# Optimization experiments

Hardware: AMD Instinct MI355X
Metric: run time of the kernel (lower is better)

The kernel has to match this reference:

```python
import jax, jax.numpy as jnp
import numpy as np

N_NODES = 102400   # 256 graphs x 400 nodes
N_EDGES = 1638400  # avg degree 16
C_IN = 128
C_OUT = 128
N_SAGE = 3         # gnn_num
G = 256            # num graphs
M = 400            # nodes per graph (equal-sized -> to_dense_batch is a reshape)


def setup_inputs() -> dict:
    key = jax.random.key(0)
    ks = jax.random.split(key, 6)
    x = jax.random.normal(ks[0], (N_NODES, C_IN), dtype=jnp.float32)
    edge_index = jax.random.randint(ks[1], (2, N_EDGES), 0, N_NODES, dtype=jnp.int32)
    # nodes sorted by graph id, equal graph sizes (matches to_dense_batch assumptions)
    batch = (jnp.arange(N_NODES, dtype=jnp.int32) // M)
    s_in = 1.0 / np.sqrt(C_IN)
    s_out = 1.0 / np.sqrt(C_OUT)
    W_g = jax.random.normal(ks[2], (C_IN, C_OUT), dtype=jnp.float32) * s_in
    b_g = jnp.zeros((C_OUT,), dtype=jnp.float32)
    W_l = jax.random.normal(ks[3], (N_SAGE, C_OUT, C_OUT), dtype=jnp.float32) * s_out  # neighbor lin
    b_l = jnp.zeros((N_SAGE, C_OUT), dtype=jnp.float32)
    W_r = jax.random.normal(ks[4], (N_SAGE, C_OUT, C_OUT), dtype=jnp.float32) * s_out  # root lin (no bias in PyG)
    return {"x": x, "W_g": W_g, "b_g": b_g, "W_l": W_l, "b_l": b_l,
            "W_r": W_r, "edge_index": edge_index, "batch": batch}


def _gcn_conv(x, W, b, src, dst):
    # PyG GCNConv: h = x W; add self loops; norm = d^{-1/2}_src * d^{-1/2}_dst,
    # deg = in-degree at dst counting the self loop; aggregate at dst; add bias.
    h = x @ W                                                     # [N, C_out]
    ones = jnp.ones((N_EDGES,), dtype=h.dtype)
    deg = jax.ops.segment_sum(ones, dst, num_segments=N_NODES) + 1.0
    dinv = jax.lax.rsqrt(deg)                                     # [N]
    norm = dinv[src] * dinv[dst]                                  # [E]
    agg = jax.ops.segment_sum(h[src] * norm[:, None], dst, num_segments=N_NODES)
    agg = agg + h * (dinv * dinv)[:, None]                        # self-loop term
    return agg + b


def _sage_conv(x, W_l, b_l, W_r, src, dst):
    # PyG SAGEConv (mean aggr): out = mean_{j in N(i)} x_j @ W_l + b_l + x @ W_r
    ones = jnp.ones((N_EDGES,), dtype=x.dtype)
    cnt = jax.ops.segment_sum(ones, dst, num_segments=N_NODES)
    s = jax.ops.segment_sum(x[src], dst, num_segments=N_NODES)
    mean = s / jnp.maximum(cnt, 1.0)[:, None]
    return mean @ W_l + b_l + x @ W_r


def _to_dense(x):
    # equal-sized graphs with nodes sorted by batch -> to_dense_batch == reshape
    return x.reshape(G, M, C_OUT)


def reference(x, W_g, b_g, W_l, b_l, W_r, edge_index, batch):
    src, dst = edge_index[0], edge_index[1]
    x = jax.nn.relu(_gcn_conv(x, W_g, b_g, src, dst))
    outs = [_to_dense(x)]
    for i in range(N_SAGE):
        x = jax.nn.relu(_sage_conv(x, W_l[i], b_l[i], W_r[i], src, dst))
        outs.append(_to_dense(x))
    return jnp.stack(outs)  # [N_SAGE+1, G, M, C_OUT]
```

## Files before the change

kernel.cpp:

```cpp
#include <hip/hip_runtime.h>

#define C 128
#define SLOT 64
typedef __attribute__((ext_vector_type(8))) short bf16x8;
typedef __attribute__((ext_vector_type(4))) float f32x4;

__device__ __forceinline__ unsigned short f2bf_rtn(float f) {
    unsigned u = __float_as_uint(f);
    return (unsigned short)((u + 0x7fff + ((u >> 16) & 1)) >> 16);
}
__device__ __forceinline__ float bflo(unsigned u) { return __uint_as_float(u << 16); }
__device__ __forceinline__ float bfhi(unsigned u) { return __uint_as_float(u & 0xffff0000u); }

__device__ __forceinline__ void gload_lds16(const unsigned short* g, unsigned short* l) {
    __builtin_amdgcn_global_load_lds(
        (const __attribute__((address_space(1))) void*)g,
        (__attribute__((address_space(3))) void*)l, 16, 0, 0);
}

__device__ __forceinline__ void split_bf16(float w, unsigned short& hb, unsigned short& lb) {
    unsigned u = __float_as_uint(w);
    hb = (unsigned short)(u >> 16);
    float hf = __uint_as_float(u & 0xffff0000u);
    lb = (unsigned short)(__float_as_uint(w - hf) >> 16);
}

__global__ __launch_bounds__(256) void wprep_all(const float* __restrict__ Wg,
        const float* __restrict__ Wl, const float* __restrict__ Wr,
        unsigned short* __restrict__ dstG, unsigned short* __restrict__ dstF) {
    int idx = blockIdx.x * 256 + threadIdx.x;
    if (idx < 16384) {
        int k64 = idx & 63, ch = (idx >> 6) & 127, chunk = idx >> 13;
        int k = chunk * 64 + k64;
        unsigned short hb, lb;
        split_bf16(Wg[(size_t)k * 128 + ch], hb, lb);
        int pos = (((k64 >> 3) ^ (ch & 7)) << 3) | (k64 & 7);
        size_t base = ((size_t)chunk * 2) * 8192 + ch * 64 + pos;
        dstG[base] = hb;
        dstG[base + 8192] = lb;
        return;
    }
    idx -= 16384;
    if (idx >= 3 * 4 * 128 * 64) return;
    int k64 = idx & 63, ch = (idx >> 6) & 127, chunk = (idx >> 13) & 3, layer = idx >> 15;
    int k = chunk * 64 + k64;
    float w = (k < 128) ? Wl[((size_t)layer * 128 + k) * 128 + ch]
                        : Wr[((size_t)layer * 128 + (k - 128)) * 128 + ch];
    unsigned short hb, lb;
    split_bf16(w, hb, lb);
    int pos = (((k64 >> 3) ^ (ch & 7)) << 3) | (k64 & 7);
    size_t base = (((size_t)layer * 4 + chunk) * 2) * 8192 + ch * 64 + pos;
    dstF[base] = hb;
    dstF[base + 8192] = lb;
}

__global__ __launch_bounds__(256) void build_gemm_kernel(
        const int* __restrict__ ei, int* __restrict__ deg, int* __restrict__ rank, int E,
        const float* __restrict__ x, const unsigned short* __restrict__ Wp,
        unsigned short* __restrict__ outbf) {
    __shared__ unsigned short Bs[2][128][64];
    const int b2 = blockIdx.x >> 1;
    const int t = threadIdx.x;

    if (!(blockIdx.x & 1)) {
        const int base = b2 * 1024 + t * 4;
        int4 d4 = *(const int4*)(ei + E + base);
        int4 r;
        r.x = atomicAdd(&deg[d4.x], 1);
        r.y = atomicAdd(&deg[d4.y], 1);
        r.z = atomicAdd(&deg[d4.z], 1);
        r.w = atomicAdd(&deg[d4.w], 1);
        *(int4*)(rank + base) = r;
        return;
    }

    unsigned short* BsFlat = &Bs[0][0][0];
    const int lane = t & 63;
    const int wv = t >> 6;
    const int rowbase = b2 * 64 + wv * 16;
    const int arow = rowbase + (lane & 15);
    const int kq = lane >> 4;

    f32x4 acc[8];
#pragma unroll
    for (int f = 0; f < 8; f++) acc[f] = (f32x4){0.f, 0.f, 0.f, 0.f};

#pragma unroll
    for (int c = 0; c < 2; c++) {
        __syncthreads();
        {
            const unsigned short* srcW = Wp + (size_t)c * 16384;
#pragma unroll
            for (int i = 0; i < 8; i++)
                gload_lds16(srcW + (wv * 8 + i) * 512 + lane * 8,
                            BsFlat + (wv * 8 + i) * 512);
        }
        bf16x8 Ah[2], Al[2];
#pragma unroll
        for (int j = 0; j < 2; j++) {
            const float* base = x + (size_t)arow * C + c * 64 + j * 32;
            float4 x0 = ((const float4*)base)[kq * 2];
            float4 x1 = ((const float4*)base)[kq * 2 + 1];
            float xv[8] = {x0.x, x0.y, x0.z, x0.w, x1.x, x1.y, x1.z, x1.w};
#pragma unroll
            for (int q = 0; q < 8; q++) {
                unsigned u = __float_as_uint(xv[q]);
                Ah[j][q] = (short)(u >> 16);
                float hf = __uint_as_float(u & 0xffff0000u);
                Al[j][q] = (short)(__float_as_uint(xv[q] - hf) >> 16);
            }
        }
        __syncthreads();
#pragma unroll
        for (int j = 0; j < 2; j++) {
#pragma unroll
            for (int f = 0; f < 8; f++) {
                const int chh = f * 16 + (lane & 15);
                const int uu = (j * 4 + kq) ^ (lane & 7);
                bf16x8 bh = *(const bf16x8*)&Bs[0][chh][uu * 8];
                bf16x8 bl = *(const bf16x8*)&Bs[1][chh][uu * 8];
                acc[f] = __builtin_amdgcn_mfma_f32_16x16x32_bf16(Ah[j], bh, acc[f], 0, 0, 0);
                acc[f] = __builtin_amdgcn_mfma_f32_16x16x32_bf16(Al[j], bh, acc[f], 0, 0, 0);
                acc[f] = __builtin_amdgcn_mfma_f32_16x16x32_bf16(Ah[j], bl, acc[f], 0, 0, 0);
            }
        }
    }
    const int col = lane & 15;
    const int rq = lane >> 4;
#pragma unroll
    for (int f = 0; f < 8; f++)
#pragma unroll
        for (int j = 0; j < 4; j++) {
            const size_t o = (size_t)(rowbase + rq * 4 + j) * C + f * 16 + col;
            outbf[o] = f2bf_rtn(acc[f][j]);
        }
}

__global__ __launch_bounds__(256) void scatter_scale_kernel(
        const int* __restrict__ ei, const int* __restrict__ rank,
        int* __restrict__ csr, int E, const int* __restrict__ deg,
        unsigned short* __restrict__ tbl, float* __restrict__ dinv,
        float* __restrict__ cinv, int n) {
    const int SB = E >> 10;
    const int t = threadIdx.x;
    if (blockIdx.x < SB) {
        const int base = blockIdx.x * 1024 + t * 4;
        int4 s4 = *(const int4*)(ei + base);
        int4 d4 = *(const int4*)(ei + E + base);
        int4 r4 = *(const int4*)(rank + base);
        if (r4.x < SLOT) csr[(d4.x << 6) + r4.x] = s4.x;
        if (r4.y < SLOT) csr[(d4.y << 6) + r4.y] = s4.y;
        if (r4.z < SLOT) csr[(d4.z << 6) + r4.z] = s4.z;
        if (r4.w < SLOT) csr[(d4.w << 6) + r4.w] = s4.w;
        return;
    }
    const int rb = (blockIdx.x - SB) * 16 + (t >> 4);
    if (rb >= n) return;
    const int ch = (t & 15) * 8;
    const int d = deg[rb];
    const float di = rsqrtf((float)(d + 1));
    if ((t & 15) == 0) {
        dinv[rb] = di;
        cinv[rb] = 1.0f / (float)max(d, 1);
    }
    unsigned short* row = tbl + (size_t)rb * C + ch;
    uint4 v = *(const uint4*)row;
    uint4 w;
    w.x = (unsigned)f2bf_rtn(bflo(v.x) * di) | ((unsigned)f2bf_rtn(bfhi(v.x) * di) << 16);
    w.y = (unsigned)f2bf_rtn(bflo(v.y) * di) | ((unsigned)f2bf_rtn(bfhi(v.y) * di) << 16);
    w.z = (unsigned)f2bf_rtn(bflo(v.z) * di) | ((unsigned)f2bf_rtn(bfhi(v.z) * di) << 16);
    w.w = (unsigned)f2bf_rtn(bflo(v.w) * di) | ((unsigned)f2bf_rtn(bfhi(v.w) * di) << 16);
    *(uint4*)row = w;
}

template<int WBF>
__global__ __launch_bounds__(256) void gemm_sage(
        const unsigned short* __restrict__ Xbf, const unsigned short* __restrict__ Mbf,
        const unsigned short* __restrict__ Wp, const float* __restrict__ bias,
        float* __restrict__ outf, unsigned short* __restrict__ outbf) {
    __shared__ unsigned short Bs[2][128][64];
    unsigned short* BsFlat = &Bs[0][0][0];
    const int t = threadIdx.x;
    const int lane = t & 63;
    const int wv = t >> 6;
    const int rowbase = blockIdx.x * 64 + wv * 16;
    const int arow = rowbase + (lane & 15);
    const int kq = lane >> 4;

    f32x4 acc[8];
#pragma unroll
    for (int f = 0; f < 8; f++) acc[f] = (f32x4){0.f, 0.f, 0.f, 0.f};

#pragma unroll
    for (int c = 0; c < 4; c++) {
        __syncthreads();
        {
            const unsigned short* srcW = Wp + (size_t)c * 16384;
#pragma unroll
            for (int i = 0; i < 8; i++)
                gload_lds16(srcW + (wv * 8 + i) * 512 + lane * 8,
                            BsFlat + (wv * 8 + i) * 512);
        }
        const unsigned short* tab = (c < 2) ? Mbf : Xbf;
        bf16x8 Ah[2];
#pragma unroll
        for (int j = 0; j < 2; j++)
            Ah[j] = *(const bf16x8*)(tab + (size_t)arow * C + (c & 1) * 64 + j * 32 + kq * 8);
        __syncthreads();
#pragma unroll
        for (int j = 0; j < 2; j++) {
#pragma unroll
            for (int f = 0; f < 8; f++) {
                const int chh = f * 16 + (lane & 15);
                const int uu = (j * 4 + kq) ^ (lane & 7);
                bf16x8 bh = *(const bf16x8*)&Bs[0][chh][uu * 8];
                bf16x8 bl = *(const bf16x8*)&Bs[1][chh][uu * 8];
                acc[f] = __builtin_amdgcn_mfma_f32_16x16x32_bf16(Ah[j], bh, acc[f], 0, 0, 0);
                acc[f] = __builtin_amdgcn_mfma_f32_16x16x32_bf16(Ah[j], bl, acc[f], 0, 0, 0);
            }
        }
    }
    const int col = lane & 15;
    const int rq = lane >> 4;
#pragma unroll
    for (int f = 0; f < 8; f++) {
        const float b = bias[f * 16 + col];
#pragma unroll
        for (int j = 0; j < 4; j++) {
            const size_t o = (size_t)(rowbase + rq * 4 + j) * C + f * 16 + col;
            float v = fmaxf(acc[f][j] + b, 0.f);
            outf[o] = v;
            if (WBF) outbf[o] = f2bf_rtn(v);
        }
    }
}

template<int SELF, int BIASRELU, int WF, int WBF>
__global__ __launch_bounds__(256) void agg_kernel(
        const unsigned short* __restrict__ tbl, const int* __restrict__ csr,
        const int* __restrict__ deg, const float* __restrict__ scale,
        const float* __restrict__ bias, float* __restrict__ outf,
        unsigned short* __restrict__ outbf, int n) {
    const int lane = threadIdx.x & 63;
    const int half = lane >> 5, li = lane & 31;
    const int i = blockIdx.x * 8 + (threadIdx.x >> 6) * 2 + half;
    if (i >= n) return;
    const int dcount = min(deg[i], SLOT);
    const int b = i << 6;
    const int c4 = li * 4;
    float a0 = 0.f, a1 = 0.f, a2 = 0.f, a3 = 0.f;
    for (int base = 0; base < dcount; base += 32) {
        const int cnt = min(32, dcount - base);
        int idx = (base + li < dcount) ? csr[b + base + li] : 0;
        int p = 0;
        for (; p + 8 <= cnt; p += 8) {
            int s0 = __shfl(idx, half * 32 + p);
            int s1 = __shfl(idx, half * 32 + p + 1);
            int s2 = __shfl(idx, half * 32 + p + 2);
            int s3 = __shfl(idx, half * 32 + p + 3);
            int s4 = __shfl(idx, half * 32 + p + 4);
            int s5 = __shfl(idx, half * 32 + p + 5);
            int s6 = __shfl(idx, half * 32 + p + 6);
            int s7 = __shfl(idx, half * 32 + p + 7);
            uint2 v0 = *(const uint2*)(tbl + (size_t)s0 * C + c4);
            uint2 v1 = *(const uint2*)(tbl + (size_t)s1 * C + c4);
            uint2 v2 = *(const uint2*)(tbl + (size_t)s2 * C + c4);
            uint2 v3 = *(const uint2*)(tbl + (size_t)s3 * C + c4);
            uint2 v4 = *(const uint2*)(tbl + (size_t)s4 * C + c4);
            uint2 v5 = *(const uint2*)(tbl + (size_t)s5 * C + c4);
            uint2 v6 = *(const uint2*)(tbl + (size_t)s6 * C + c4);
            uint2 v7 = *(const uint2*)(tbl + (size_t)s7 * C + c4);
            a0 += bflo(v0.x) + bflo(v1.x) + bflo(v2.x) + bflo(v3.x)
                + bflo(v4.x) + bflo(v5.x) + bflo(v6.x) + bflo(v7.x);
            a1 += bfhi(v0.x) + bfhi(v1.x) + bfhi(v2.x) + bfhi(v3.x)
                + bfhi(v4.x) + bfhi(v5.x) + bfhi(v6.x) + bfhi(v7.x);
            a2 += bflo(v0.y) + bflo(v1.y) + bflo(v2.y) + bflo(v3.y)
                + bflo(v4.y) + bflo(v5.y) + bflo(v6.y) + bflo(v7.y);
            a3 += bfhi(v0.y) + bfhi(v1.y) + bfhi(v2.y) + bfhi(v3.y)
                + bfhi(v4.y) + bfhi(v5.y) + bfhi(v6.y) + bfhi(v7.y);
        }
        for (; p + 4 <= cnt; p += 4) {
            int s0 = __shfl(idx, half * 32 + p);
            int s1 = __shfl(idx, half * 32 + p + 1);
            int s2 = __shfl(idx, half * 32 + p + 2);
            int s3 = __shfl(idx, half * 32 + p + 3);
            uint2 v0 = *(const uint2*)(tbl + (size_t)s0 * C + c4);
            uint2 v1 = *(const uint2*)(tbl + (size_t)s1 * C + c4);
            uint2 v2 = *(const uint2*)(tbl + (size_t)s2 * C + c4);
            uint2 v3 = *(const uint2*)(tbl + (size_t)s3 * C + c4);
            a0 += bflo(v0.x) + bflo(v1.x) + bflo(v2.x) + bflo(v3.x);
            a1 += bfhi(v0.x) + bfhi(v1.x) + bfhi(v2.x) + bfhi(v3.x);
            a2 += bflo(v0.y) + bflo(v1.y) + bflo(v2.y) + bflo(v3.y);
            a3 += bfhi(v0.y) + bfhi(v1.y) + bfhi(v2.y) + bfhi(v3.y);
        }
        for (; p < cnt; p++) {
            int s = __shfl(idx, half * 32 + p);
            uint2 v = *(const uint2*)(tbl + (size_t)s * C + c4);
            a0 += bflo(v.x); a1 += bfhi(v.x);
            a2 += bflo(v.y); a3 += bfhi(v.y);
        }
    }
    if (SELF) {
        uint2 h = *(const uint2*)(tbl + (size_t)i * C + c4);
        a0 += bflo(h.x); a1 += bfhi(h.x);
        a2 += bflo(h.y); a3 += bfhi(h.y);
    }
    const float sc = scale[i];
    a0 *= sc; a1 *= sc; a2 *= sc; a3 *= sc;
    if (BIASRELU) {
        float4 bb = *(const float4*)(bias + c4);
        a0 = fmaxf(a0 + bb.x, 0.f);
        a1 = fmaxf(a1 + bb.y, 0.f);
        a2 = fmaxf(a2 + bb.z, 0.f);
        a3 = fmaxf(a3 + bb.w, 0.f);
    }
    if (WF) {
        float4 r; r.x = a0; r.y = a1; r.z = a2; r.w = a3;
        *(float4*)(outf + (size_t)i * C + c4) = r;
    }
    if (WBF) {
        uint2 pk;
        pk.x = (unsigned)f2bf_rtn(a0) | ((unsigned)f2bf_rtn(a1) << 16);
        pk.y = (unsigned)f2bf_rtn(a2) | ((unsigned)f2bf_rtn(a3) << 16);
        *(uint2*)(outbf + (size_t)i * C + c4) = pk;
    }
}


extern "C" void kernel_launch(void* const* d_in, const int* in_sizes, int n_in,
                              void* d_out, int out_size, void* d_ws, size_t ws_size,
                              hipStream_t stream) {
    const float* x   = (const float*)d_in[0];
    const float* W_g = (const float*)d_in[1];
    const float* b_g = (const float*)d_in[2];
    const float* W_l = (const float*)d_in[3];
    const float* b_l = (const float*)d_in[4];
    const float* W_r = (const float*)d_in[5];
    const int*   ei  = (const int*)d_in[6];

    const int N = in_sizes[0] / C;
    const int E = in_sizes[6] / 2;
    const size_t NC = (size_t)N * C;

    char* ws = (char*)d_ws;
    unsigned short* meanbf = (unsigned short*)ws;
    int* rank = (int*)meanbf;
    unsigned short* tblA   = meanbf + NC;
    unsigned short* tblB   = tblA + NC;
    int* deg  = (int*)(tblB + NC);
    float* dinv = (float*)(deg + N);
    float* cinv = dinv + N;
    unsigned short* wsWg = (unsigned short*)(cinv + N);
    unsigned short* wsWf = wsWg + 32768;

    float* out0 = (float*)d_out;
    int* csr = (int*)(out0 + 3 * NC);

    hipMemsetAsync(deg, 0, (size_t)N * 4, stream);
    wprep_all<<<448, 256, 0, stream>>>(W_g, W_l, W_r, wsWg, wsWf);

    build_gemm_kernel<<<2 * (N / 64), 256, 0, stream>>>(ei, deg, rank, E,
                                                        x, wsWg, tblA);
    scatter_scale_kernel<<<(E >> 10) + N / 16, 256, 0, stream>>>(
        ei, rank, csr, E, deg, tblA, dinv, cinv, N);

    agg_kernel<1, 1, 1, 1><<<(N + 7) / 8, 256, 0, stream>>>(tblA, csr, deg, dinv,
                                                            b_g, out0, tblB, N);

    const unsigned short* tin[3] = {tblB, tblA, tblB};
    unsigned short* tout[3] = {tblA, tblB, nullptr};
    for (int l = 0; l < 3; l++) {
        float* yout = out0 + (size_t)(l + 1) * NC;
        agg_kernel<0, 0, 0, 1><<<(N + 7) / 8, 256, 0, stream>>>(
            tin[l], csr, deg, cinv, nullptr, nullptr, meanbf, N);
        if (l < 2)
            gemm_sage<1><<<N / 64, 256, 0, stream>>>(tin[l], meanbf,
                wsWf + (size_t)l * 65536, b_l + (size_t)l * C, yout, tout[l]);
        else
            gemm_sage<0><<<N / 64, 256, 0, stream>>>(tin[l], meanbf,
                wsWf + (size_t)l * 65536, b_l + (size_t)l * C, yout, nullptr);
    }
}
```

Measured before the change: 424.5 us.

## Widen neighbor gathers, drop bf16 low-part weights in SAGE GEMM, fold deg memset

The aggregation kernel now gives each node 16 lanes that each load 16 bytes per neighbor row, instead of 32 lanes loading 8 bytes. That handles four nodes per wave and issues fewer, wider gather loads. The SAGE GEMM keeps only the high bf16 part of each weight rather than the hi/lo split, which halves the MFMA count and the weight LDS traffic at some cost in accuracy. The degree-array memset moves into the weight-prep kernel, removing one separate operation.

```diff
diff --git a/kernel.cpp b/kernel.cpp
--- a/kernel.cpp
+++ b/kernel.cpp
@@ -27,8 +27,10 @@
 
 __global__ __launch_bounds__(256) void wprep_all(const float* __restrict__ Wg,
         const float* __restrict__ Wl, const float* __restrict__ Wr,
-        unsigned short* __restrict__ dstG, unsigned short* __restrict__ dstF) {
+        unsigned short* __restrict__ dstG, unsigned short* __restrict__ dstF,
+        int* __restrict__ deg, int n) {
     int idx = blockIdx.x * 256 + threadIdx.x;
+    if (idx < n) deg[idx] = 0;
     if (idx < 16384) {
         int k64 = idx & 63, ch = (idx >> 6) & 127, chunk = idx >> 13;
         int k = chunk * 64 + k64;
@@ -38,20 +40,17 @@
         size_t base = ((size_t)chunk * 2) * 8192 + ch * 64 + pos;
         dstG[base] = hb;
         dstG[base + 8192] = lb;
-        return;
-    }
-    idx -= 16384;
-    if (idx >= 3 * 4 * 128 * 64) return;
-    int k64 = idx & 63, ch = (idx >> 6) & 127, chunk = (idx >> 13) & 3, layer = idx >> 15;
-    int k = chunk * 64 + k64;
-    float w = (k < 128) ? Wl[((size_t)layer * 128 + k) * 128 + ch]
-                        : Wr[((size_t)layer * 128 + (k - 128)) * 128 + ch];
-    unsigned short hb, lb;
-    split_bf16(w, hb, lb);
-    int pos = (((k64 >> 3) ^ (ch & 7)) << 3) | (k64 & 7);
-    size_t base = (((size_t)layer * 4 + chunk) * 2) * 8192 + ch * 64 + pos;
-    dstF[base] = hb;
-    dstF[base + 8192] = lb;
+    }
+    int fidx = idx - 16384;
+    if (fidx >= 0 && fidx < 3 * 4 * 128 * 64) {
+        int k64 = fidx & 63, ch = (fidx >> 6) & 127, chunk = (fidx >> 13) & 3,
+            layer = fidx >> 15;
+        int k = chunk * 64 + k64;
+        float w = (k < 128) ? Wl[((size_t)layer * 128 + k) * 128 + ch]
+                            : Wr[((size_t)layer * 128 + (k - 128)) * 128 + ch];
+        int pos = (((k64 >> 3) ^ (ch & 7)) << 3) | (k64 & 7);
+        dstF[(((size_t)layer * 4 + chunk)) * 8192 + ch * 64 + pos] = f2bf_rtn(w);
+    }
 }
 
 __global__ __launch_bounds__(256) void build_gemm_kernel(
@@ -178,8 +177,8 @@
         const unsigned short* __restrict__ Xbf, const unsigned short* __restrict__ Mbf,
         const unsigned short* __restrict__ Wp, const float* __restrict__ bias,
         float* __restrict__ outf, unsigned short* __restrict__ outbf) {
-    __shared__ unsigned short Bs[2][128][64];
-    unsigned short* BsFlat = &Bs[0][0][0];
+    __shared__ unsigned short Bs[128][64];
+    unsigned short* BsFlat = &Bs[0][0];
     const int t = threadIdx.x;
     const int lane = t & 63;
     const int wv = t >> 6;
@@ -195,11 +194,11 @@
     for (int c = 0; c < 4; c++) {
         __syncthreads();
         {
-            const unsigned short* srcW = Wp + (size_t)c * 16384;
-#pragma unroll
-            for (int i = 0; i < 8; i++)
-                gload_lds16(srcW + (wv * 8 + i) * 512 + lane * 8,
-                            BsFlat + (wv * 8 + i) * 512);
+            const unsigned short* srcW = Wp + (size_t)c * 8192;
+#pragma unroll
+            for (int i = 0; i < 4; i++)
+                gload_lds16(srcW + (wv * 4 + i) * 512 + lane * 8,
+                            BsFlat + (wv * 4 + i) * 512);
         }
         const unsigned short* tab = (c < 2) ? Mbf : Xbf;
         bf16x8 Ah[2];
@@ -213,10 +212,8 @@
             for (int f = 0; f < 8; f++) {
                 const int chh = f * 16 + (lane & 15);
                 const int uu = (j * 4 + kq) ^ (lane & 7);
-                bf16x8 bh = *(const bf16x8*)&Bs[0][chh][uu * 8];
-                bf16x8 bl = *(const bf16x8*)&Bs[1][chh][uu * 8];
+                bf16x8 bh = *(const bf16x8*)&Bs[chh][uu * 8];
                 acc[f] = __builtin_amdgcn_mfma_f32_16x16x32_bf16(Ah[j], bh, acc[f], 0, 0, 0);
-                acc[f] = __builtin_amdgcn_mfma_f32_16x16x32_bf16(Ah[j], bl, acc[f], 0, 0, 0);
             }
         }
     }
@@ -242,87 +239,88 @@
         const float* __restrict__ bias, float* __restrict__ outf,
         unsigned short* __restrict__ outbf, int n) {
     const int lane = threadIdx.x & 63;
-    const int half = lane >> 5, li = lane & 31;
-    const int i = blockIdx.x * 8 + (threadIdx.x >> 6) * 2 + half;
+    const int qi = lane & 15;
+    const int i = blockIdx.x * 16 + (threadIdx.x >> 6) * 4 + (lane >> 4);
     if (i >= n) return;
     const int dcount = min(deg[i], SLOT);
     const int b = i << 6;
-    const int c4 = li * 4;
+    const int c8 = qi * 8;
     float a0 = 0.f, a1 = 0.f, a2 = 0.f, a3 = 0.f;
-    for (int base = 0; base < dcount; base += 32) {
-        const int cnt = min(32, dcount - base);
-        int idx = (base + li < dcount) ? csr[b + base + li] : 0;
+    float a4 = 0.f, a5 = 0.f, a6 = 0.f, a7 = 0.f;
+#define ACC8(v) do { \
+        a0 += bflo(v.x); a1 += bfhi(v.x); a2 += bflo(v.y); a3 += bfhi(v.y); \
+        a4 += bflo(v.z); a5 += bfhi(v.z); a6 += bflo(v.w); a7 += bfhi(v.w); } while (0)
+    for (int base = 0; base < dcount; base += 16) {
+        const int cnt = min(16, dcount - base);
+        int idx = (base + qi < dcount) ? csr[b + base + qi] : 0;
         int p = 0;
         for (; p + 8 <= cnt; p += 8) {
-            int s0 = __shfl(idx, half * 32 + p);
-            int s1 = __shfl(idx, half * 32 + p + 1);
-            int s2 = __shfl(idx, half * 32 + p + 2);
-            int s3 = __shfl(idx, half * 32 + p + 3);
-            int s4 = __shfl(idx, half * 32 + p + 4);
-            int s5 = __shfl(idx, half * 32 + p + 5);
-            int s6 = __shfl(idx, half * 32 + p + 6);
-            int s7 = __shfl(idx, half * 32 + p + 7);
-            uint2 v0 = *(const uint2*)(tbl + (size_t)s0 * C + c4);
-            uint2 v1 = *(const uint2*)(tbl + (size_t)s1 * C + c4);
-            uint2 v2 = *(const uint2*)(tbl + (size_t)s2 * C + c4);
-            uint2 v3 = *(const uint2*)(tbl + (size_t)s3 * C + c4);
-            uint2 v4 = *(const uint2*)(tbl + (size_t)s4 * C + c4);
-            uint2 v5 = *(const uint2*)(tbl + (size_t)s5 * C + c4);
-            uint2 v6 = *(const uint2*)(tbl + (size_t)s6 * C + c4);
-            uint2 v7 = *(const uint2*)(tbl + (size_t)s7 * C + c4);
-            a0 += bflo(v0.x) + bflo(v1.x) + bflo(v2.x) + bflo(v3.x)
-                + bflo(v4.x) + bflo(v5.x) + bflo(v6.x) + bflo(v7.x);
-            a1 += bfhi(v0.x) + bfhi(v1.x) + bfhi(v2.x) + bfhi(v3.x)
-                + bfhi(v4.x) + bfhi(v5.x) + bfhi(v6.x) + bfhi(v7.x);
-            a2 += bflo(v0.y) + bflo(v1.y) + bflo(v2.y) + bflo(v3.y)
-                + bflo(v4.y) + bflo(v5.y) + bflo(v6.y) + bflo(v7.y);
-            a3 += bfhi(v0.y) + bfhi(v1.y) + bfhi(v2.y) + bfhi(v3.y)
-                + bfhi(v4.y) + bfhi(v5.y) + bfhi(v6.y) + bfhi(v7.y);
+            int s0 = __shfl(idx, (lane & 48) + p);
+            int s1 = __shfl(idx, (lane & 48) + p + 1);
+            int s2 = __shfl(idx, (lane & 48) + p + 2);
+            int s3 = __shfl(idx, (lane & 48) + p + 3);
+            int s4 = __shfl(idx, (lane & 48) + p + 4);
+            int s5 = __shfl(idx, (lane & 48) + p + 5);
+            int s6 = __shfl(idx, (lane & 48) + p + 6);
+            int s7 = __shfl(idx, (lane & 48) + p + 7);
+            uint4 v0 = *(const uint4*)(tbl + (size_t)s0 * C + c8);
+            uint4 v1 = *(const uint4*)(tbl + (size_t)s1 * C + c8);
+            uint4 v2 = *(const uint4*)(tbl + (size_t)s2 * C + c8);
+            uint4 v3 = *(const uint4*)(tbl + (size_t)s3 * C + c8);
+            uint4 v4 = *(const uint4*)(tbl + (size_t)s4 * C + c8);
+            uint4 v5 = *(const uint4*)(tbl + (size_t)s5 * C + c8);
+            uint4 v6 = *(const uint4*)(tbl + (size_t)s6 * C + c8);
+            uint4 v7 = *(const uint4*)(tbl + (size_t)s7 * C + c8);
+            ACC8(v0); ACC8(v1); ACC8(v2); ACC8(v3);
+            ACC8(v4); ACC8(v5); ACC8(v6); ACC8(v7);
         }
         for (; p + 4 <= cnt; p += 4) {
-            int s0 = __shfl(idx, half * 32 + p);
-            int s1 = __shfl(idx, half * 32 + p + 1);
-            int s2 = __shfl(idx, half * 32 + p + 2);
-            int s3 = __shfl(idx, half * 32 + p + 3);
-            uint2 v0 = *(const uint2*)(tbl + (size_t)s0 * C + c4);
-            uint2 v1 = *(const uint2*)(tbl + (size_t)s1 * C + c4);
-            uint2 v2 = *(const uint2*)(tbl + (size_t)s2 * C + c4);
-            uint2 v3 = *(const uint2*)(tbl + (size_t)s3 * C + c4);
-            a0 += bflo(v0.x) + bflo(v1.x) + bflo(v2.x) + bflo(v3.x);
-            a1 += bfhi(v0.x) + bfhi(v1.x) + bfhi(v2.x) + bfhi(v3.x);
-            a2 += bflo(v0.y) + bflo(v1.y) + bflo(v2.y) + bflo(v3.y);
-            a3 += bfhi(v0.y) + bfhi(v1.y) + bfhi(v2.y) + bfhi(v3.y);
+            int s0 = __shfl(idx, (lane & 48) + p);
+            int s1 = __shfl(idx, (lane & 48) + p + 1);
+            int s2 = __shfl(idx, (lane & 48) + p + 2);
+            int s3 = __shfl(idx, (lane & 48) + p + 3);
+            uint4 v0 = *(const uint4*)(tbl + (size_t)s0 * C + c8);
+            uint4 v1 = *(const uint4*)(tbl + (size_t)s1 * C + c8);
+            uint4 v2 = *(const uint4*)(tbl + (size_t)s2 * C + c8);
+            uint4 v3 = *(const uint4*)(tbl + (size_t)s3 * C + c8);
+            ACC8(v0); ACC8(v1); ACC8(v2); ACC8(v3);
         }
         for (; p < cnt; p++) {
-            int s = __shfl(idx, half * 32 + p);
-            uint2 v = *(const uint2*)(tbl + (size_t)s * C + c4);
-            a0 += bflo(v.x); a1 += bfhi(v.x);
-            a2 += bflo(v.y); a3 += bfhi(v.y);
-        }
-    }
+            int s = __shfl(idx, (lane & 48) + p);
+            uint4 v = *(const uint4*)(tbl + (size_t)s * C + c8);
+            ACC8(v);
+        }
+    }
+#undef ACC8
     if (SELF) {
-        uint2 h = *(const uint2*)(tbl + (size_t)i * C + c4);
-        a0 += bflo(h.x); a1 += bfhi(h.x);
-        a2 += bflo(h.y); a3 += bfhi(h.y);
+        uint4 h = *(const uint4*)(tbl + (size_t)i * C + c8);
+        a0 += bflo(h.x); a1 += bfhi(h.x); a2 += bflo(h.y); a3 += bfhi(h.y);
+        a4 += bflo(h.z); a5 += bfhi(h.z); a6 += bflo(h.w); a7 += bfhi(h.w);
     }
     const float sc = scale[i];
     a0 *= sc; a1 *= sc; a2 *= sc; a3 *= sc;
+    a4 *= sc; a5 *= sc; a6 *= sc; a7 *= sc;
     if (BIASRELU) {
-        float4 bb = *(const float4*)(bias + c4);
-        a0 = fmaxf(a0 + bb.x, 0.f);
-        a1 = fmaxf(a1 + bb.y, 0.f);
-        a2 = fmaxf(a2 + bb.z, 0.f);
-        a3 = fmaxf(a3 + bb.w, 0.f);
+        float4 b0 = *(const float4*)(bias + c8);
+        float4 b1 = *(const float4*)(bias + c8 + 4);
+        a0 = fmaxf(a0 + b0.x, 0.f); a1 = fmaxf(a1 + b0.y, 0.f);
+        a2 = fmaxf(a2 + b0.z, 0.f); a3 = fmaxf(a3 + b0.w, 0.f);
+        a4 = fmaxf(a4 + b1.x, 0.f); a5 = fmaxf(a5 + b1.y, 0.f);
+        a6 = fmaxf(a6 + b1.z, 0.f); a7 = fmaxf(a7 + b1.w, 0.f);
     }
     if (WF) {
-        float4 r; r.x = a0; r.y = a1; r.z = a2; r.w = a3;
-        *(float4*)(outf + (size_t)i * C + c4) = r;
+        float4 r0; r0.x = a0; r0.y = a1; r0.z = a2; r0.w = a3;
+        float4 r1; r1.x = a4; r1.y = a5; r1.z = a6; r1.w = a7;
+        *(float4*)(outf + (size_t)i * C + c8) = r0;
+        *(float4*)(outf + (size_t)i * C + c8 + 4) = r1;
     }
     if (WBF) {
-        uint2 pk;
+        uint4 pk;
         pk.x = (unsigned)f2bf_rtn(a0) | ((unsigned)f2bf_rtn(a1) << 16);
         pk.y = (unsigned)f2bf_rtn(a2) | ((unsigned)f2bf_rtn(a3) << 16);
-        *(uint2*)(outbf + (size_t)i * C + c4) = pk;
+        pk.z = (unsigned)f2bf_rtn(a4) | ((unsigned)f2bf_rtn(a5) << 16);
+        pk.w = (unsigned)f2bf_rtn(a6) | ((unsigned)f2bf_rtn(a7) << 16);
+        *(uint4*)(outbf + (size_t)i * C + c8) = pk;
     }
 }
 
@@ -356,28 +354,27 @@
     float* out0 = (float*)d_out;
     int* csr = (int*)(out0 + 3 * NC);
 
-    hipMemsetAsync(deg, 0, (size_t)N * 4, stream);
-    wprep_all<<<448, 256, 0, stream>>>(W_g, W_l, W_r, wsWg, wsWf);
+    wprep_all<<<448, 256, 0, stream>>>(W_g, W_l, W_r, wsWg, wsWf, deg, N);
 
     build_gemm_kernel<<<2 * (N / 64), 256, 0, stream>>>(ei, deg, rank, E,
                                                         x, wsWg, tblA);
     scatter_scale_kernel<<<(E >> 10) + N / 16, 256, 0, stream>>>(
         ei, rank, csr, E, deg, tblA, dinv, cinv, N);
 
-    agg_kernel<1, 1, 1, 1><<<(N + 7) / 8, 256, 0, stream>>>(tblA, csr, deg, dinv,
-                                                            b_g, out0, tblB, N);
+    agg_kernel<1, 1, 1, 1><<<(N + 15) / 16, 256, 0, stream>>>(tblA, csr, deg, dinv,
+                                                              b_g, out0, tblB, N);
 
     const unsigned short* tin[3] = {tblB, tblA, tblB};
     unsigned short* tout[3] = {tblA, tblB, nullptr};
     for (int l = 0; l < 3; l++) {
         float* yout = out0 + (size_t)(l + 1) * NC;
-        agg_kernel<0, 0, 0, 1><<<(N + 7) / 8, 256, 0, stream>>>(
+        agg_kernel<0, 0, 0, 1><<<(N + 15) / 16, 256, 0, stream>>>(
             tin[l], csr, deg, cinv, nullptr, nullptr, meanbf, N);
         if (l < 2)
             gemm_sage<1><<<N / 64, 256, 0, stream>>>(tin[l], meanbf,
-                wsWf + (size_t)l * 65536, b_l + (size_t)l * C, yout, tout[l]);
+                wsWf + (size_t)l * 32768, b_l + (size_t)l * C, yout, tout[l]);
         else
             gemm_sage<0><<<N / 64, 256, 0, stream>>>(tin[l], meanbf,
-                wsWf + (size_t)l * 65536, b_l + (size_t)l * C, yout, nullptr);
-    }
-}
+                wsWf + (size_t)l * 32768, b_l + (size_t)l * C, yout, nullptr);
+    }
+}
```

New measurement: 421.6 us (median of 2 runs). Within noise of the previous version (-0.7%).
